# Kernel optimization log

Measured on AMD Instinct MI355X. Metric: run time of the kernel, lower is better.

## Reference

```python
import jax, jax.numpy as jnp
import numpy as np

B, T, N_EMBD = 1, 2048, 2048
N_HEAD = 16
KV_LOW = 512      # kv_low_rank == head_size (compressed value dim)
Q_LOW = 1024
ROPE_HS = 64
QK_HS = KV_LOW + ROPE_HS  # 576
HEAD_SIZE = KV_LOW        # v_equiv = c_kv.view(B,1,T,head_size)


def _rope_tables(seq_len, dim, base=10000.0):
    # litgpt-style: theta over half dim, duplicated to full dim
    inv = 1.0 / (base ** (np.arange(0, dim, 2, dtype=np.float32) / dim))
    t = np.arange(seq_len, dtype=np.float32)
    freqs = np.outer(t, inv)                      # [T, dim/2]
    emb = np.concatenate([freqs, freqs], axis=-1)  # [T, dim]
    return jnp.asarray(np.cos(emb)), jnp.asarray(np.sin(emb))


def _apply_rope(x, cos, sin):
    # x: [..., T, d]; cos/sin broadcastable [T, d]. rotate-half RoPE.
    d = x.shape[-1]
    x1, x2 = x[..., : d // 2], x[..., d // 2:]
    rotated = jnp.concatenate([-x2, x1], axis=-1)
    return x * cos + rotated * sin


def setup_inputs() -> dict:
    key = jax.random.key(0)
    ks = jax.random.split(key, 4)
    x = jax.random.normal(ks[0], (B, T, N_EMBD), dtype=jnp.float32)
    cos, sin = _rope_tables(T, ROPE_HS)
    s = 0.02
    W_qkv = jax.random.normal(ks[1], (N_EMBD, KV_LOW + ROPE_HS + Q_LOW), dtype=jnp.float32) * s
    W_qdec = jax.random.normal(ks[2], (Q_LOW, N_HEAD * QK_HS), dtype=jnp.float32) * s
    W_out = jax.random.normal(ks[3], (N_HEAD * HEAD_SIZE, N_EMBD), dtype=jnp.float32) * s
    return {"x": x, "cos": cos, "sin": sin, "W_qkv": W_qkv, "W_qdec": W_qdec, "W_out": W_out}


def reference(x, cos, sin, W_qkv, W_qdec, W_out):
    Bq, Tq, _ = x.shape
    # latent encoding and split
    latents = x @ W_qkv                                       # [B,T,kv+rope+q]
    c_kv = latents[..., :KV_LOW]                              # [B,T,512] (keys-nope and values)
    k_r = latents[..., KV_LOW:KV_LOW + ROPE_HS]               # [B,T,64]
    c_q = latents[..., KV_LOW + ROPE_HS:]                     # [B,T,1024]
    # per-head query decode
    q = (c_q @ W_qdec).reshape(Bq, Tq, N_HEAD, QK_HS)         # [B,T,H,576]
    q_nope, q_r = q[..., :KV_LOW], q[..., KV_LOW:]
    # partial RoPE
    k_r = _apply_rope(k_r, cos, sin)                          # [B,T,64]
    q_r = _apply_rope(q_r, cos[None, :, None, :], sin[None, :, None, :])  # [B,T,H,64]
    q = jnp.concatenate([q_nope, q_r], axis=-1)               # [B,T,H,576]
    q = jnp.swapaxes(q, 1, 2)                                 # [B,H,T,576]
    k = jnp.concatenate([c_kv, k_r], axis=-1)                 # [B,T,576] shared across heads
    v = c_kv                                                  # [B,T,512] shared across heads
    scale = 1.0 / jnp.sqrt(jnp.float32(HEAD_SIZE))
    scores = jnp.einsum('bhtd,bsd->bhts', q, k) * scale       # [B,H,T,T]
    causal = jnp.tril(jnp.ones((Tq, Tq), dtype=bool))
    scores = jnp.where(causal, scores, jnp.finfo(scores.dtype).min)
    attn = jax.nn.softmax(scores, axis=-1)
    y = jnp.einsum('bhts,bsd->bhtd', attn, v)                 # [B,H,T,512]
    y = jnp.swapaxes(y, 1, 2).reshape(Bq, Tq, N_HEAD * HEAD_SIZE)
    return y @ W_out                                          # [B,T,n_embd]
```

## Files before the change

### kernel.cpp

```cpp
#include <hip/hip_runtime.h>

typedef __bf16 bf16x8_t __attribute__((ext_vector_type(8)));
typedef float f32x4_t __attribute__((ext_vector_type(4)));

#define LAT_LD 1664
#define QK_DIM 576
#define V_DIM 512
#define NHEAD 16
#define TSEQ 2048
#define QLD 9216
#define YLD 8192
#define KLD 576
#define SCALE 0.044194173824159216f

__device__ __forceinline__ unsigned short f2bf(float f) {
  union { float f; unsigned int u; } v; v.f = f;
  unsigned int r = v.u + 0x7FFFu + ((v.u >> 16) & 1u);
  return (unsigned short)(r >> 16);
}

__device__ __forceinline__ void load_lds16(const unsigned short* g, unsigned short* l) {
  __builtin_amdgcn_global_load_lds((const __attribute__((address_space(1))) void*)g,
                                   (__attribute__((address_space(3))) void*)l, 16, 0, 0);
}

__device__ __forceinline__ void conv_t_body(const float* __restrict__ src, int R, int Csrc,
                                            unsigned short* __restrict__ dst,
                                            int bx, int by, int tid,
                                            unsigned short (*T)[72]) {
  const int r0 = bx * 64, c0 = by * 64;
  const bool live = (c0 < Csrc);
#pragma unroll
  for (int it = 0; it < 4; ++it) {
    int idx = it * 256 + tid;
    int r = idx >> 4, c4 = (idx & 15) * 4;
    float4 v = {0.f, 0.f, 0.f, 0.f};
    if (live) v = *(const float4*)&src[(size_t)(r0 + r) * Csrc + c0 + c4];
    T[c4 + 0][r] = f2bf(v.x);
    T[c4 + 1][r] = f2bf(v.y);
    T[c4 + 2][r] = f2bf(v.z);
    T[c4 + 3][r] = f2bf(v.w);
  }
  __syncthreads();
#pragma unroll
  for (int it = 0; it < 2; ++it) {
    int idx = it * 256 + tid;
    int cc = idx >> 3, r8 = (idx & 7) * 8;
    uint4 v = *(const uint4*)&T[cc][r8];
    *(uint4*)&dst[(size_t)(c0 + cc) * R + r0 + r8] = v;
  }
}

__global__ __launch_bounds__(256) void prep_all(
    const float* __restrict__ x, unsigned short* __restrict__ xb,
    const float* __restrict__ wqkv, unsigned short* __restrict__ wqkvT,
    const float* __restrict__ wqdec, unsigned short* __restrict__ wqdecT,
    const float* __restrict__ wout, unsigned short* __restrict__ woutT,
    float* __restrict__ lsum) {
  __shared__ unsigned short T[64][72];
  const int blk = blockIdx.x, tid = threadIdx.x;
  if (blk < 4096) {
    int i = (blk * 256 + tid) * 4;
    float4 v = *(const float4*)&x[i];
    ushort4 o;
    o.x = f2bf(v.x); o.y = f2bf(v.y); o.z = f2bf(v.z); o.w = f2bf(v.w);
    *(ushort4*)&xb[i] = o;
  } else if (blk < 4928) {
    int l = blk - 4096;
    conv_t_body(wqkv, 2048, 1600, wqkvT, l & 31, l >> 5, tid, T);
  } else if (blk < 7232) {
    int l = blk - 4928;
    conv_t_body(wqdec, 1024, 9216, wqdecT, l & 15, l >> 4, tid, T);
  } else if (blk < 11328) {
    int l = blk - 7232;
    conv_t_body(wout, 8192, 2048, woutT, l & 127, l >> 7, tid, T);
  } else {
    int i = ((blk - 11328) * 256 + tid) * 4;
    *(float4*)&lsum[i] = (float4){0.f, 0.f, 0.f, 0.f};
  }
}

__global__ __launch_bounds__(256) void postlat(
    const float* __restrict__ P1,
    unsigned short* __restrict__ lat,
    unsigned short* __restrict__ kbuf,
    unsigned short* __restrict__ vtg,
    const float* __restrict__ cosb, const float* __restrict__ sinb) {
  __shared__ unsigned short T[64][72];
  const int tid = threadIdx.x;
  const int bx = blockIdx.x, by = blockIdx.y;
  const int r0 = bx * 64, c0 = by * 64;
  const size_t n = (size_t)2048 * 1664;

#pragma unroll
  for (int it = 0; it < 4; ++it) {
    int idx = it * 256 + tid;
    int r = idx >> 4, c4 = (idx & 15) * 4;
    size_t off = (size_t)(r0 + r) * 1664 + c0 + c4;
    float4 a = *(const float4*)&P1[off];
    float4 b = *(const float4*)&P1[n + off];
    ushort4 o;
    o.x = f2bf(a.x + b.x); o.y = f2bf(a.y + b.y);
    o.z = f2bf(a.z + b.z); o.w = f2bf(a.w + b.w);
    if (by < 8) {
      *(ushort4*)&kbuf[(size_t)(r0 + r) * KLD + c0 + c4] = o;
      T[c4 + 0][r] = o.x; T[c4 + 1][r] = o.y; T[c4 + 2][r] = o.z; T[c4 + 3][r] = o.w;
    } else if (by == 8) {
      T[r][c4 + 0] = o.x; T[r][c4 + 1] = o.y; T[r][c4 + 2] = o.z; T[r][c4 + 3] = o.w;
    } else {
      *(ushort4*)&lat[(size_t)(r0 + r) * LAT_LD + c0 + c4] = o;
    }
  }
  if (by > 8) return;
  __syncthreads();
  if (by < 8) {
#pragma unroll
    for (int it = 0; it < 2; ++it) {
      int idx = it * 256 + tid;
      int cc = idx >> 3, r8 = (idx & 7) * 8;
      uint4 v = *(const uint4*)&T[cc][r8];
      *(uint4*)&vtg[(size_t)(c0 + cc) * TSEQ + r0 + r8] = v;
    }
  } else {
#pragma unroll
    for (int it = 0; it < 8; ++it) {
      int idx = it * 256 + tid;
      int r = idx >> 5, d = idx & 31;
      int t = r0 + r;
      union { unsigned int u; float f; } a, b;
      a.u = ((unsigned int)T[r][d]) << 16;
      b.u = ((unsigned int)T[r][d + 32]) << 16;
      float c0f = cosb[t * 64 + d], s0f = sinb[t * 64 + d];
      float c1f = cosb[t * 64 + d + 32], s1f = sinb[t * 64 + d + 32];
      kbuf[(size_t)t * KLD + 512 + d] = f2bf(a.f * c0f - b.f * s0f);
      kbuf[(size_t)t * KLD + 544 + d] = f2bf(b.f * c1f + a.f * s1f);
    }
  }
}

#define GEMM_PROLOGUE()                                                     \
  __shared__ __align__(16) unsigned short As[8192];                         \
  __shared__ __align__(16) unsigned short Bs[8192];                         \
  const int tid = threadIdx.x;                                              \
  const int wave = tid >> 6, lane = tid & 63;                               \
  const int quad = lane >> 4, l16 = lane & 15;                              \
  const int wm = wave >> 1, wn = wave & 1;                                  \
  f32x4_t acc[4][4];                                                        \
  f32x4_t zero = {0.f, 0.f, 0.f, 0.f};                                      \
  _Pragma("unroll") for (int mi = 0; mi < 4; ++mi)                          \
    _Pragma("unroll") for (int ni = 0; ni < 4; ++ni) acc[mi][ni] = zero;

#define GEMM_KLOOP(Aptr, Alda, Bptr, Bldb, M0, N0, KLEN)                    \
  for (int k0 = 0; k0 < (KLEN); k0 += 64) {                                 \
    _Pragma("unroll") for (int p2 = 0; p2 < 2; ++p2) {                      \
      int ci = p2 * 256 + tid;                                              \
      int rr2 = ci >> 2, cc2 = (ci & 3) * 8;                                \
      const unsigned short* ga = &(Aptr)[(size_t)((M0) + rr2) * (Alda) + k0 + cc2]; \
      const unsigned short* gb = &(Bptr)[(size_t)((N0) + rr2) * (Bldb) + k0 + cc2]; \
      load_lds16(ga,      &As[ci * 8]);                                     \
      load_lds16(ga + 32, &As[4096 + ci * 8]);                              \
      load_lds16(gb,      &Bs[ci * 8]);                                     \
      load_lds16(gb + 32, &Bs[4096 + ci * 8]);                              \
    }                                                                       \
    __syncthreads();                                                        \
    _Pragma("unroll") for (int hf = 0; hf < 2; ++hf) {                      \
      bf16x8_t af[4], bfr[4];                                               \
      _Pragma("unroll") for (int mi = 0; mi < 4; ++mi)                      \
        af[mi] = *(const bf16x8_t*)&As[hf * 4096 + (wm * 64 + mi * 16 + l16) * 32 + quad * 8]; \
      _Pragma("unroll") for (int ni = 0; ni < 4; ++ni)                      \
        bfr[ni] = *(const bf16x8_t*)&Bs[hf * 4096 + (wn * 64 + ni * 16 + l16) * 32 + quad * 8]; \
      _Pragma("unroll") for (int mi = 0; mi < 4; ++mi)                      \
        _Pragma("unroll") for (int ni = 0; ni < 4; ++ni)                    \
          acc[mi][ni] = __builtin_amdgcn_mfma_f32_16x16x32_bf16(af[mi], bfr[ni], acc[mi][ni], 0, 0, 0); \
    }                                                                       \
    __syncthreads();                                                        \
  }

__global__ __launch_bounds__(256, 2) void gemm_splitk(
    const unsigned short* __restrict__ A, int lda,
    const unsigned short* __restrict__ Bt, int ldb,
    float* __restrict__ P, int ldc, int Ks) {
  const int m0 = blockIdx.y * 128, n0 = blockIdx.x * 128;
  const size_t koff = (size_t)blockIdx.z * Ks;
  const unsigned short* Ap = A + koff;
  const unsigned short* Bp = Bt + koff;
  float* C = P + (size_t)blockIdx.z * ((size_t)gridDim.y * 128) * ldc;
  GEMM_PROLOGUE();
  GEMM_KLOOP(Ap, lda, Bp, ldb, m0, n0, Ks);
#pragma unroll
  for (int mi = 0; mi < 4; ++mi)
#pragma unroll
    for (int ni = 0; ni < 4; ++ni)
#pragma unroll
      for (int r = 0; r < 4; ++r) {
        int row = m0 + wm * 64 + mi * 16 + quad * 4 + r;
        int col = n0 + wn * 64 + ni * 16 + l16;
        C[(size_t)row * ldc + col] = acc[mi][ni][r];
      }
}

#define SWZ(o) ((o) ^ ((((o) >> 9) & 1) << 5))
#define SBAR() do { __builtin_amdgcn_s_barrier(); __builtin_amdgcn_sched_barrier(0); } while (0)
#define VMCNT(n) asm volatile("s_waitcnt vmcnt(" #n ")" ::: "memory")

__device__ __forceinline__ bf16x8_t frag_ld256(const unsigned short* region, int rl, int kk, int quad) {
  int lin = rl * 128 + kk * 64 + quad * 16;
  lin ^= ((rl >> 2) & 1) << 5;
  return *(const bf16x8_t*)((const unsigned char*)region + lin);
}

#define MFMAQ(MB, NB, BREG)                                                 \
  __builtin_amdgcn_s_setprio(1);                                            \
  _Pragma("unroll") for (int mi = 0; mi < 4; ++mi)                          \
    _Pragma("unroll") for (int ni = 0; ni < 2; ++ni)                        \
      _Pragma("unroll") for (int kk = 0; kk < 2; ++kk)                      \
        acc[(MB) + mi][(NB) + ni] = __builtin_amdgcn_mfma_f32_16x16x32_bf16( \
            a[mi][kk], BREG[ni][kk], acc[(MB) + mi][(NB) + ni], 0, 0, 0);    \
  __builtin_amdgcn_s_setprio(0);

__device__ __forceinline__ void kloop256(
    const unsigned short* __restrict__ A, int lda, int m0,
    const unsigned short* __restrict__ Bt, int ldb, int n0,
    int NT, unsigned short* lds, f32x4_t (&acc)[8][4],
    int tid, int quad, int l16, int wm, int wn) {
  const int o0 = tid * 16, o1 = 8192 + tid * 16;
  const int so0 = SWZ(o0), so1 = SWZ(o1);
  const int srow0 = so0 >> 7, scol0 = (so0 & 127) >> 1;
  const int srow1 = so1 >> 7, scol1 = (so1 & 127) >> 1;
  auto STG = [&](int k, int r) {
    if (k >= NT) return;
    unsigned short* dst = lds + ((k & 1) << 15) + (r << 13);
    const unsigned short* g = (r < 2) ? A : Bt;
    const int ld = (r < 2) ? lda : ldb;
    const int rb = ((r < 2) ? m0 : n0) + (r & 1) * 128;
    const int c0 = k * 64;
    load_lds16(g + (size_t)(rb + srow0) * ld + c0 + scol0, dst + tid * 8);
    load_lds16(g + (size_t)(rb + srow1) * ld + c0 + scol1, dst + 4096 + tid * 8);
  };
  STG(0, 0); STG(0, 1); STG(0, 2); STG(0, 3);
  STG(1, 2); STG(1, 0);
  VMCNT(4);
  SBAR();
  const int brow = (wn & 1) * 64;
  for (int t = 0; t < NT; ++t) {
    const unsigned short* Ar = lds + ((t & 1) << 15) + (wm << 13);
    const unsigned short* Br = lds + ((t & 1) << 15) + 16384 + ((wn >> 1) << 13);
    bf16x8_t a[4][2], b0[2][2], b1[2][2];
#pragma unroll
    for (int mi = 0; mi < 4; ++mi) {
      a[mi][0] = frag_ld256(Ar, mi * 16 + l16, 0, quad);
      a[mi][1] = frag_ld256(Ar, mi * 16 + l16, 1, quad);
    }
#pragma unroll
    for (int ni = 0; ni < 2; ++ni) {
      b0[ni][0] = frag_ld256(Br, brow + ni * 16 + l16, 0, quad);
      b0[ni][1] = frag_ld256(Br, brow + ni * 16 + l16, 1, quad);
    }
    STG(t + 1, 1);
    SBAR();
    MFMAQ(0, 0, b0);
    SBAR();
#pragma unroll
    for (int ni = 0; ni < 2; ++ni) {
      b1[ni][0] = frag_ld256(Br, brow + (2 + ni) * 16 + l16, 0, quad);
      b1[ni][1] = frag_ld256(Br, brow + (2 + ni) * 16 + l16, 1, quad);
    }
    STG(t + 1, 3);
    SBAR();
    MFMAQ(0, 2, b1);
    SBAR();
#pragma unroll
    for (int mi = 0; mi < 4; ++mi) {
      a[mi][0] = frag_ld256(Ar, (4 + mi) * 16 + l16, 0, quad);
      a[mi][1] = frag_ld256(Ar, (4 + mi) * 16 + l16, 1, quad);
    }
    STG(t + 2, 2);
    SBAR();
    MFMAQ(4, 2, b1);
    SBAR();
    STG(t + 2, 0);
    SBAR();
    MFMAQ(4, 0, b0);
    if (t < NT - 2) { VMCNT(4); }
    else if (t == NT - 2) { VMCNT(0); }
    SBAR();
  }
}

__global__ __launch_bounds__(512, 2) void gemm256_splitk(
    const unsigned short* __restrict__ A, int lda,
    const unsigned short* __restrict__ Bt, int ldb,
    float* __restrict__ P, int ldc, int Ks) {
  __shared__ __align__(16) unsigned short lds[65536];
  const int tid = threadIdx.x;
  const int quad = (tid >> 4) & 3, l16 = tid & 15;
  const int wave = tid >> 6, wm = wave >> 2, wn = wave & 3;
  const int m0 = blockIdx.y * 256, n0 = blockIdx.x * 256;
  const unsigned short* Ap = A + (size_t)blockIdx.z * Ks;
  const unsigned short* Bp = Bt + (size_t)blockIdx.z * Ks;
  float* C = P + (size_t)blockIdx.z * ((size_t)gridDim.y * 256) * ldc;
  f32x4_t acc[8][4];
  f32x4_t z4 = {0.f, 0.f, 0.f, 0.f};
#pragma unroll
  for (int mi = 0; mi < 8; ++mi)
#pragma unroll
    for (int ni = 0; ni < 4; ++ni) acc[mi][ni] = z4;
  kloop256(Ap, lda, m0, Bp, ldb, n0, Ks >> 6, lds, acc, tid, quad, l16, wm, wn);
#pragma unroll
  for (int mi = 0; mi < 8; ++mi)
#pragma unroll
    for (int ni = 0; ni < 4; ++ni)
#pragma unroll
      for (int r = 0; r < 4; ++r) {
        const int row = m0 + wm * 128 + mi * 16 + quad * 4 + r;
        const int col = n0 + wn * 64 + ni * 16 + l16;
        C[(size_t)row * ldc + col] = acc[mi][ni][r];
      }
}

__global__ __launch_bounds__(512, 2) void gemm256_qdec(
    const unsigned short* __restrict__ A,
    const unsigned short* __restrict__ Bt,
    unsigned short* __restrict__ qbuf,
    const float* __restrict__ cosb, const float* __restrict__ sinb) {
  __shared__ __align__(16) unsigned short lds[65536];
  const int tid = threadIdx.x;
  const int quad = (tid >> 4) & 3, l16 = tid & 15;
  const int wave = tid >> 6, wm = wave >> 2, wn = wave & 3;
  const int d = blockIdx.y * gridDim.x + blockIdx.x;
  const int wg = (d & 7) * 36 + (d >> 3);
  const int m0 = (wg / 36) * 256, n0 = (wg % 36) * 256;
  f32x4_t acc[8][4];
  f32x4_t z4 = {0.f, 0.f, 0.f, 0.f};
#pragma unroll
  for (int mi = 0; mi < 8; ++mi)
#pragma unroll
    for (int ni = 0; ni < 4; ++ni) acc[mi][ni] = z4;
  kloop256(A, LAT_LD, m0, Bt, 1024, n0, 16, lds, acc, tid, quad, l16, wm, wn);

  const int cb = n0 + wn * 64;
  const bool ropeh = (cb % QK_DIM) == 512;
#pragma unroll
  for (int mi = 0; mi < 8; ++mi)
#pragma unroll
    for (int r = 0; r < 4; ++r) {
      const int t = m0 + wm * 128 + mi * 16 + quad * 4 + r;
      if (ropeh) {
#pragma unroll
        for (int ni = 0; ni < 2; ++ni) {
          const int dd = ni * 16 + l16;
          float c0f = cosb[t * 64 + dd], s0f = sinb[t * 64 + dd];
          float c1f = cosb[t * 64 + dd + 32], s1f = sinb[t * 64 + dd + 32];
          float v1 = acc[mi][ni][r], v2 = acc[mi][ni + 2][r];
          qbuf[(size_t)t * QLD + cb + dd] = f2bf(v1 * c0f - v2 * s0f);
          qbuf[(size_t)t * QLD + cb + 32 + dd] = f2bf(v2 * c1f + v1 * s1f);
        }
      } else {
#pragma unroll
        for (int ni = 0; ni < 4; ++ni)
          qbuf[(size_t)t * QLD + cb + ni * 16 + l16] = f2bf(acc[mi][ni][r]);
      }
    }
}

__global__ __launch_bounds__(256) void reduce4_f32(const float* __restrict__ p,
                                                   float* __restrict__ dst, int n) {
  int i = (blockIdx.x * 256 + threadIdx.x) * 4;
  if (i < n) {
    float4 a = *(const float4*)&p[i];
    float4 b = *(const float4*)&p[(size_t)n + i];
    float4 c = *(const float4*)&p[2 * (size_t)n + i];
    float4 d = *(const float4*)&p[3 * (size_t)n + i];
    float4 o;
    o.x = (a.x + b.x) + (c.x + d.x);
    o.y = (a.y + b.y) + (c.y + d.y);
    o.z = (a.z + b.z) + (c.z + d.z);
    o.w = (a.w + b.w) + (c.w + d.w);
    *(float4*)&dst[i] = o;
  }
}

__global__ __launch_bounds__(256, 2) void qke_kernel(
    const unsigned short* __restrict__ qbuf,
    const unsigned short* __restrict__ kbuf,
    unsigned short* __restrict__ Ebuf,
    float* __restrict__ lsum, int hbase) {
  int tx = blockIdx.x, ig = 15, cnt = 16;
  while (tx >= cnt) { tx -= cnt; --ig; --cnt; }
  const int j = tx;
  const int hl = blockIdx.y, h = hbase + hl;
  const int Kmax = (ig + 1) << 7;
  const int r0g = ig << 7;
  const int pre = (ig * (ig + 1)) >> 1;

  const unsigned short* A = qbuf + (size_t)r0g * QLD + h * QK_DIM;
  const unsigned short* Bt = kbuf + (size_t)(j << 7) * KLD;
  unsigned short* Eh = Ebuf + ((size_t)hl * 136 + pre) * 16384;

  GEMM_PROLOGUE();
  GEMM_KLOOP(A, QLD, Bt, KLD, 0, 0, QK_DIM);

#pragma unroll
  for (int mi = 0; mi < 4; ++mi) {
    float rs[4] = {0.f, 0.f, 0.f, 0.f};
#pragma unroll
    for (int ni = 0; ni < 4; ++ni)
#pragma unroll
      for (int r = 0; r < 4; ++r) {
        int qr = r0g + wm * 64 + mi * 16 + quad * 4 + r;
        int key = (j << 7) + wn * 64 + ni * 16 + l16;
        float e = (key <= qr) ? __expf(acc[mi][ni][r] * SCALE) : 0.f;
        rs[r] += e;
        Eh[(size_t)(qr - r0g) * Kmax + key] = f2bf(e);
      }
#pragma unroll
    for (int r = 0; r < 4; ++r) {
      float s = rs[r];
#pragma unroll
      for (int off = 1; off < 16; off <<= 1) s += __shfl_xor(s, off, 64);
      if (l16 == 0) {
        int qr = r0g + wm * 64 + mi * 16 + quad * 4 + r;
        atomicAdd(&lsum[h * TSEQ + qr], s);
      }
    }
  }
}

__global__ __launch_bounds__(256, 2) void pv_kernel(
    const unsigned short* __restrict__ Ebuf,
    const unsigned short* __restrict__ vtg,
    const float* __restrict__ lsum,
    unsigned short* __restrict__ ybuf, int hbase) {
  const int ig = 15 - blockIdx.y;
  const int hl = blockIdx.z, h = hbase + hl;
  const int n0 = blockIdx.x * 128;
  const int Kmax = (ig + 1) << 7;
  const int pre = (ig * (ig + 1)) >> 1;

  const unsigned short* A = Ebuf + ((size_t)hl * 136 + pre) * 16384;

  GEMM_PROLOGUE();
  GEMM_KLOOP(A, Kmax, vtg, TSEQ, 0, n0, Kmax);

#pragma unroll
  for (int mi = 0; mi < 4; ++mi)
#pragma unroll
    for (int r = 0; r < 4; ++r) {
      int row_g = (ig << 7) + wm * 64 + mi * 16 + quad * 4 + r;
      float inv = 1.f / lsum[h * TSEQ + row_g];
#pragma unroll
      for (int ni = 0; ni < 4; ++ni) {
        int col = h * V_DIM + n0 + wn * 64 + ni * 16 + l16;
        ybuf[(size_t)row_g * YLD + col] = f2bf(acc[mi][ni][r] * inv);
      }
    }
}

extern "C" void kernel_launch(void* const* d_in, const int* in_sizes, int n_in,
                              void* d_out, int out_size, void* d_ws, size_t ws_size,
                              hipStream_t stream) {
  (void)in_sizes; (void)n_in; (void)out_size; (void)ws_size;
  const float* x     = (const float*)d_in[0];
  const float* cosb  = (const float*)d_in[1];
  const float* sinb  = (const float*)d_in[2];
  const float* wqkv  = (const float*)d_in[3];
  const float* wqdec = (const float*)d_in[4];
  const float* wout  = (const float*)d_in[5];
  float* out = (float*)d_out;

  unsigned short* ws     = (unsigned short*)d_ws;
  unsigned short* xb     = ws;
  unsigned short* wqkvT  = xb     + (size_t)2048 * 2048;
  unsigned short* wqdecT = wqkvT  + (size_t)1664 * 2048;
  unsigned short* lat    = wqdecT + (size_t)9216 * 1024;
  unsigned short* qbuf   = lat    + (size_t)2048 * 1664;
  unsigned short* woutT  = qbuf   + (size_t)2048 * 9216;
  unsigned short* ybuf   = woutT  + (size_t)2048 * 8192;
  unsigned short* vtg    = ybuf   + (size_t)2048 * 8192;
  unsigned short* kbuf   = vtg    + (size_t)512 * 2048;
  float*          lsumf  = (float*)(kbuf + (size_t)2048 * 576);
  unsigned short* Ebuf   = ws;
  float*          P1     = (float*)qbuf;
  float*          Pf     = (float*)ws;

  prep_all<<<11360, 256, 0, stream>>>(x, xb, wqkv, wqkvT, wqdec, wqdecT, wout, woutT, lsumf);

  gemm_splitk<<<dim3(13, 16, 2), 256, 0, stream>>>(xb, 2048, wqkvT, 2048, P1, 1664, 1024);
  postlat<<<dim3(32, 26), 256, 0, stream>>>(P1, lat, kbuf, vtg, cosb, sinb);

  gemm256_qdec<<<dim3(36, 8), 512, 0, stream>>>(lat + 576, wqdecT, qbuf, cosb, sinb);

  qke_kernel<<<dim3(136, 8), 256, 0, stream>>>(qbuf, kbuf, Ebuf, lsumf, 0);
  pv_kernel<<<dim3(4, 16, 8), 256, 0, stream>>>(Ebuf, vtg, lsumf, ybuf, 0);
  qke_kernel<<<dim3(136, 8), 256, 0, stream>>>(qbuf, kbuf, Ebuf, lsumf, 8);
  pv_kernel<<<dim3(4, 16, 8), 256, 0, stream>>>(Ebuf, vtg, lsumf, ybuf, 8);

  gemm256_splitk<<<dim3(8, 8, 4), 512, 0, stream>>>(ybuf, 8192, woutT, 8192, Pf, 2048, 2048);
  reduce4_f32<<<4096, 256, 0, stream>>>(Pf, out, 2048 * 2048);
}
```

Before: 511.8 us.

## Switch q-decode GEMM to 128x128 tiles and change LDS swizzle pattern

Replaces the 256x256-tile, 512-thread q-decode GEMM with a 128x128-tile, 256-thread kernel built on the generic GEMM macros, launched over a 72x16 grid. Separately, the LDS swizzle used by the remaining 256-tile kernel becomes a 3-bit XOR over 16-byte chunks, meant to cut LDS bank conflicts. The staging lambda is also moved into a helper function with a macro. Smaller tiles give more blocks and better CU fill but less data reuse per block, and the XOR order drops the grouped tile rasterization.

```diff
diff --git a/kernel.cpp b/kernel.cpp
--- a/kernel.cpp
+++ b/kernel.cpp
@@ -199,14 +199,63 @@
       }
 }
 
-#define SWZ(o) ((o) ^ ((((o) >> 9) & 1) << 5))
+__global__ __launch_bounds__(256, 2) void gemm_qdec(
+    const unsigned short* __restrict__ A,
+    const unsigned short* __restrict__ Bt,
+    unsigned short* __restrict__ qbuf,
+    const float* __restrict__ cosb, const float* __restrict__ sinb) {
+  const int m0 = blockIdx.y * 128, n0 = blockIdx.x * 128;
+  GEMM_PROLOGUE();
+  GEMM_KLOOP(A, LAT_LD, Bt, 1024, m0, n0, 1024);
+
+  const int cb = n0 + wn * 64;
+  const bool ropeh = (cb % QK_DIM) == 512;
+#pragma unroll
+  for (int mi = 0; mi < 4; ++mi)
+#pragma unroll
+    for (int r = 0; r < 4; ++r) {
+      int t = m0 + wm * 64 + mi * 16 + quad * 4 + r;
+      if (ropeh) {
+#pragma unroll
+        for (int ni = 0; ni < 2; ++ni) {
+          int d = ni * 16 + l16;
+          float c0f = cosb[t * 64 + d], s0f = sinb[t * 64 + d];
+          float c1f = cosb[t * 64 + d + 32], s1f = sinb[t * 64 + d + 32];
+          float v1 = acc[mi][ni][r], v2 = acc[mi][ni + 2][r];
+          qbuf[(size_t)t * QLD + cb + d] = f2bf(v1 * c0f - v2 * s0f);
+          qbuf[(size_t)t * QLD + cb + 32 + d] = f2bf(v2 * c1f + v1 * s1f);
+        }
+      } else {
+#pragma unroll
+        for (int ni = 0; ni < 4; ++ni)
+          qbuf[(size_t)t * QLD + cb + ni * 16 + l16] = f2bf(acc[mi][ni][r]);
+      }
+    }
+}
+
+#define SWZ(o) ((o) ^ ((((o) >> 7) & 7) << 4))
 #define SBAR() do { __builtin_amdgcn_s_barrier(); __builtin_amdgcn_sched_barrier(0); } while (0)
 #define VMCNT(n) asm volatile("s_waitcnt vmcnt(" #n ")" ::: "memory")
 
 __device__ __forceinline__ bf16x8_t frag_ld256(const unsigned short* region, int rl, int kk, int quad) {
   int lin = rl * 128 + kk * 64 + quad * 16;
-  lin ^= ((rl >> 2) & 1) << 5;
+  lin ^= (rl & 7) << 4;
   return *(const bf16x8_t*)((const unsigned char*)region + lin);
+}
+
+__device__ __forceinline__ void stg256(
+    const unsigned short* __restrict__ A, int lda, int m0,
+    const unsigned short* __restrict__ Bt, int ldb, int n0,
+    unsigned short* lds, int k, int r, int NT,
+    int srow0, int scol0, int srow1, int scol1, int tid) {
+  if (k >= NT) return;
+  unsigned short* dst = lds + ((k & 1) << 15) + (r << 13);
+  const unsigned short* g = (r < 2) ? A : Bt;
+  const int ld = (r < 2) ? lda : ldb;
+  const int rb = ((r < 2) ? m0 : n0) + (r & 1) * 128;
+  const int c0 = k * 64;
+  load_lds16(g + (size_t)(rb + srow0) * ld + c0 + scol0, dst + tid * 8);
+  load_lds16(g + (size_t)(rb + srow1) * ld + c0 + scol1, dst + 4096 + tid * 8);
 }
 
 #define MFMAQ(MB, NB, BREG)                                                 \
@@ -217,6 +266,8 @@
         acc[(MB) + mi][(NB) + ni] = __builtin_amdgcn_mfma_f32_16x16x32_bf16( \
             a[mi][kk], BREG[ni][kk], acc[(MB) + mi][(NB) + ni], 0, 0, 0);    \
   __builtin_amdgcn_s_setprio(0);
+
+#define STG(k, r) stg256(A, lda, m0, Bt, ldb, n0, lds, (k), (r), NT, srow0, scol0, srow1, scol1, tid)
 
 __device__ __forceinline__ void kloop256(
     const unsigned short* __restrict__ A, int lda, int m0,
@@ -227,16 +278,6 @@
   const int so0 = SWZ(o0), so1 = SWZ(o1);
   const int srow0 = so0 >> 7, scol0 = (so0 & 127) >> 1;
   const int srow1 = so1 >> 7, scol1 = (so1 & 127) >> 1;
-  auto STG = [&](int k, int r) {
-    if (k >= NT) return;
-    unsigned short* dst = lds + ((k & 1) << 15) + (r << 13);
-    const unsigned short* g = (r < 2) ? A : Bt;
-    const int ld = (r < 2) ? lda : ldb;
-    const int rb = ((r < 2) ? m0 : n0) + (r & 1) * 128;
-    const int c0 = k * 64;
-    load_lds16(g + (size_t)(rb + srow0) * ld + c0 + scol0, dst + tid * 8);
-    load_lds16(g + (size_t)(rb + srow1) * ld + c0 + scol1, dst + 4096 + tid * 8);
-  };
   STG(0, 0); STG(0, 1); STG(0, 2); STG(0, 3);
   STG(1, 2); STG(1, 0);
   VMCNT(4);
@@ -318,51 +359,6 @@
       }
 }
 
-__global__ __launch_bounds__(512, 2) void gemm256_qdec(
-    const unsigned short* __restrict__ A,
-    const unsigned short* __restrict__ Bt,
-    unsigned short* __restrict__ qbuf,
-    const float* __restrict__ cosb, const float* __restrict__ sinb) {
-  __shared__ __align__(16) unsigned short lds[65536];
-  const int tid = threadIdx.x;
-  const int quad = (tid >> 4) & 3, l16 = tid & 15;
-  const int wave = tid >> 6, wm = wave >> 2, wn = wave & 3;
-  const int d = blockIdx.y * gridDim.x + blockIdx.x;
-  const int wg = (d & 7) * 36 + (d >> 3);
-  const int m0 = (wg / 36) * 256, n0 = (wg % 36) * 256;
-  f32x4_t acc[8][4];
-  f32x4_t z4 = {0.f, 0.f, 0.f, 0.f};
-#pragma unroll
-  for (int mi = 0; mi < 8; ++mi)
-#pragma unroll
-    for (int ni = 0; ni < 4; ++ni) acc[mi][ni] = z4;
-  kloop256(A, LAT_LD, m0, Bt, 1024, n0, 16, lds, acc, tid, quad, l16, wm, wn);
-
-  const int cb = n0 + wn * 64;
-  const bool ropeh = (cb % QK_DIM) == 512;
-#pragma unroll
-  for (int mi = 0; mi < 8; ++mi)
-#pragma unroll
-    for (int r = 0; r < 4; ++r) {
-      const int t = m0 + wm * 128 + mi * 16 + quad * 4 + r;
-      if (ropeh) {
-#pragma unroll
-        for (int ni = 0; ni < 2; ++ni) {
-          const int dd = ni * 16 + l16;
-          float c0f = cosb[t * 64 + dd], s0f = sinb[t * 64 + dd];
-          float c1f = cosb[t * 64 + dd + 32], s1f = sinb[t * 64 + dd + 32];
-          float v1 = acc[mi][ni][r], v2 = acc[mi][ni + 2][r];
-          qbuf[(size_t)t * QLD + cb + dd] = f2bf(v1 * c0f - v2 * s0f);
-          qbuf[(size_t)t * QLD + cb + 32 + dd] = f2bf(v2 * c1f + v1 * s1f);
-        }
-      } else {
-#pragma unroll
-        for (int ni = 0; ni < 4; ++ni)
-          qbuf[(size_t)t * QLD + cb + ni * 16 + l16] = f2bf(acc[mi][ni][r]);
-      }
-    }
-}
-
 __global__ __launch_bounds__(256) void reduce4_f32(const float* __restrict__ p,
                                                    float* __restrict__ dst, int n) {
   int i = (blockIdx.x * 256 + threadIdx.x) * 4;
@@ -488,7 +484,7 @@
   gemm_splitk<<<dim3(13, 16, 2), 256, 0, stream>>>(xb, 2048, wqkvT, 2048, P1, 1664, 1024);
   postlat<<<dim3(32, 26), 256, 0, stream>>>(P1, lat, kbuf, vtg, cosb, sinb);
 
-  gemm256_qdec<<<dim3(36, 8), 512, 0, stream>>>(lat + 576, wqdecT, qbuf, cosb, sinb);
+  gemm_qdec<<<dim3(72, 16), 256, 0, stream>>>(lat + 576, wqdecT, qbuf, cosb, sinb);
 
   qke_kernel<<<dim3(136, 8), 256, 0, stream>>>(qbuf, kbuf, Ebuf, lsumf, 0);
   pv_kernel<<<dim3(4, 16, 8), 256, 0, stream>>>(Ebuf, vtg, lsumf, ybuf, 0);
```

New measurement: 481.8 us. -5.9%, faster.
